# Performance work log

Measured on AMD Instinct MI355X. Metric: run time of the kernel, lower is better.

Reference implementation:

```python
import jax, jax.numpy as jnp
import numpy as np
from jax import lax


def setup_inputs() -> dict:
    key = jax.random.key(0)
    k1, k2 = jax.random.split(key)
    X = jax.random.normal(k1, (4, 32, 512, 512), dtype=jnp.float32)
    kernel = jax.random.uniform(k2, (5, 5), dtype=jnp.float32)  # torch.rand equivalent
    return {"X": X, "kernel": kernel, "stride": 1, "padding": 2}


def reference(X, kernel, stride, padding):
    # Original module: zero-pad, unfold k x k patches with given stride, and
    # compute sum(patch * kernel) for every (batch, channel, row, col) -- i.e.
    # a per-channel 2D correlation with a single shared [k, k] kernel.
    # Fold channels into the batch dim so one single-channel correlation
    # covers all of them (no cross-channel mixing in the original).
    B, C, H, W = X.shape
    k = kernel.shape[0]
    Xf = X.reshape(B * C, 1, H, W)
    out = lax.conv_general_dilated(
        Xf,
        kernel[None, None, :, :],  # OIHW = [1, 1, k, k]
        window_strides=(stride, stride),
        padding=[(padding, padding), (padding, padding)],
        dimension_numbers=("NCHW", "OIHW", "NCHW"),
    )  # lax conv is correlation (no kernel flip), matching the torch math
    _, _, Ho, Wo = out.shape
    return out.reshape(B, C, Ho, Wo)
```

## Files before the change

### kernel.cpp

```cpp
#include <hip/hip_runtime.h>

#define H 512
#define W 512
#define K 5
#define PAD 2
#define ROWS 16
#define XPT 4

typedef float vf4 __attribute__((ext_vector_type(4)));

__global__ __launch_bounds__(256) void conv5x5_kernel(
    const float* __restrict__ X, const float* __restrict__ ker,
    float* __restrict__ out)
{
    const int tx  = threadIdx.x;
    const int xb  = (blockIdx.x * 64 + tx) * XPT;
    const int y0  = blockIdx.y * (4 * ROWS) + threadIdx.y * ROWS;
    const int img = blockIdx.z;

    const float* Xp = X   + (size_t)img * H * W;
    float*       Op = out + (size_t)img * H * W;

    float kk[K][K];
    #pragma unroll
    for (int i = 0; i < K; ++i)
        #pragma unroll
        for (int j = 0; j < K; ++j)
            kk[i][j] = ker[i * K + j];

    const int q  = xb >> 2;
    const int qL = (q == 0) ? 0 : q - 1;
    const int qR = (q == W / 4 - 1) ? q : q + 1;
    const float mLo = (q == 0) ? 0.f : 1.f;
    const float mHi = (q == W / 4 - 1) ? 0.f : 1.f;

    float acc[K][XPT];
    #pragma unroll
    for (int p = 0; p < K; ++p)
        #pragma unroll
        for (int j = 0; j < XPT; ++j)
            acc[p][j] = 0.f;

    #pragma unroll
    for (int r = 0; r < ROWS + K - 1; ++r) {
        const int yr = y0 - PAD + r;
        vf4 Lv = {0.f, 0.f, 0.f, 0.f};
        vf4 Mv = {0.f, 0.f, 0.f, 0.f};
        vf4 Rv = {0.f, 0.f, 0.f, 0.f};
        if (yr >= 0 && yr < H) {
            const vf4* rp = (const vf4*)(Xp + (size_t)yr * W);
            Lv = rp[qL];
            Mv = rp[q];
            Rv = rp[qR];
        }
        float v[8];
        v[0] = Lv.z * mLo;  v[1] = Lv.w * mLo;
        v[2] = Mv.x;  v[3] = Mv.y;  v[4] = Mv.z;  v[5] = Mv.w;
        v[6] = Rv.x * mHi;  v[7] = Rv.y * mHi;

        #pragma unroll
        for (int kr = 0; kr < K; ++kr) {
            const int o = r - kr;
            if (o >= 0 && o < ROWS) {
                const int pa = o % K;
                #pragma unroll
                for (int c = 0; c < K; ++c)
                    #pragma unroll
                    for (int j = 0; j < XPT; ++j)
                        acc[pa][j] = fmaf(v[j + c], kk[kr][c], acc[pa][j]);
            }
        }

        if (r >= K - 1) {
            const int o  = r - (K - 1);
            const int pa = o % K;
            vf4 st = {acc[pa][0], acc[pa][1], acc[pa][2], acc[pa][3]};
            __builtin_nontemporal_store(st, (vf4*)(Op + (size_t)(y0 + o) * W + xb));
            #pragma unroll
            for (int j = 0; j < XPT; ++j)
                acc[pa][j] = 0.f;
        }
    }
}

extern "C" void kernel_launch(void* const* d_in, const int* in_sizes, int n_in,
                              void* d_out, int out_size, void* d_ws, size_t ws_size,
                              hipStream_t stream) {
    const float* X   = (const float*)d_in[0];
    const float* ker = (const float*)d_in[1];
    float* out = (float*)d_out;

    dim3 block(64, 4, 1);
    dim3 grid(W / (64 * XPT), H / (4 * ROWS), 4 * 32);
    hipLaunchKernelGGL(conv5x5_kernel, grid, block, 0, stream, X, ker, out);
}
```

Measured before the change: 236.8 us.

## Software-prefetch input rows into register ring buffer and halve rows per thread

Loads of upcoming input rows are issued PF rows ahead into a 4-deep register ring buffer. Out-of-range rows are clamped and then masked by multiplication rather than skipped with a branch, so loads can be issued early and overlap with the FMAs. ROWS drops from 16 to 8 and launch_bounds requests 4 blocks per CU, which raises the block count and occupancy. The cost is more halo re-reads per output row (12 loaded rows per 8 outputs instead of 20 per 16) and extra register pressure.

```diff
diff --git a/kernel.cpp b/kernel.cpp
--- a/kernel.cpp
+++ b/kernel.cpp
@@ -4,12 +4,15 @@
 #define W 512
 #define K 5
 #define PAD 2
-#define ROWS 16
+#define ROWS 8
+#define NR (ROWS + K - 1)
 #define XPT 4
+#define PF 3
+#define DEPTH 4
 
 typedef float vf4 __attribute__((ext_vector_type(4)));
 
-__global__ __launch_bounds__(256) void conv5x5_kernel(
+__global__ __launch_bounds__(256, 4) void conv5x5_kernel(
     const float* __restrict__ X, const float* __restrict__ ker,
     float* __restrict__ out)
 {
@@ -34,6 +37,16 @@
     const float mLo = (q == 0) ? 0.f : 1.f;
     const float mHi = (q == W / 4 - 1) ? 0.f : 1.f;
 
+    vf4 bl[DEPTH], bm[DEPTH], br[DEPTH];
+
+    #pragma unroll
+    for (int r = 0; r < PF; ++r) {
+        const int yr = y0 - PAD + r;
+        const int yc = yr < 0 ? 0 : (yr > H - 1 ? H - 1 : yr);
+        const vf4* rp = (const vf4*)(Xp + (size_t)yc * W);
+        bl[r] = rp[qL];  bm[r] = rp[q];  br[r] = rp[qR];
+    }
+
     float acc[K][XPT];
     #pragma unroll
     for (int p = 0; p < K; ++p)
@@ -42,21 +55,30 @@
             acc[p][j] = 0.f;
 
     #pragma unroll
-    for (int r = 0; r < ROWS + K - 1; ++r) {
+    for (int r = 0; r < NR; ++r) {
+        if (r + PF < NR) {
+            const int rr = r + PF;
+            const int yr = y0 - PAD + rr;
+            const int yc = yr < 0 ? 0 : (yr > H - 1 ? H - 1 : yr);
+            const vf4* rp = (const vf4*)(Xp + (size_t)yc * W);
+            bl[rr % DEPTH] = rp[qL];
+            bm[rr % DEPTH] = rp[q];
+            br[rr % DEPTH] = rp[qR];
+        }
+
         const int yr = y0 - PAD + r;
-        vf4 Lv = {0.f, 0.f, 0.f, 0.f};
-        vf4 Mv = {0.f, 0.f, 0.f, 0.f};
-        vf4 Rv = {0.f, 0.f, 0.f, 0.f};
-        if (yr >= 0 && yr < H) {
-            const vf4* rp = (const vf4*)(Xp + (size_t)yr * W);
-            Lv = rp[qL];
-            Mv = rp[q];
-            Rv = rp[qR];
-        }
+        const float mR = (yr >= 0 && yr < H) ? 1.f : 0.f;
+        const float mA = mLo * mR;
+        const float mC = mHi * mR;
+        const vf4 Lv = bl[r % DEPTH];
+        const vf4 Mv = bm[r % DEPTH];
+        const vf4 Rv = br[r % DEPTH];
+
         float v[8];
-        v[0] = Lv.z * mLo;  v[1] = Lv.w * mLo;
-        v[2] = Mv.x;  v[3] = Mv.y;  v[4] = Mv.z;  v[5] = Mv.w;
-        v[6] = Rv.x * mHi;  v[7] = Rv.y * mHi;
+        v[0] = Lv.z * mA;  v[1] = Lv.w * mA;
+        v[2] = Mv.x * mR;  v[3] = Mv.y * mR;
+        v[4] = Mv.z * mR;  v[5] = Mv.w * mR;
+        v[6] = Rv.x * mC;  v[7] = Rv.y * mC;
 
         #pragma unroll
         for (int kr = 0; kr < K; ++kr) {
```

After: 242.2 us. +2.3%, slower.
